# Optimization experiments

Measured on AMD Instinct MI355X. Metric: run time of the kernel, lower is better.

## Reference

```python
import jax, jax.numpy as jnp
import numpy as np
import math

B, N, L = 1, 256, 384
D_MSA, D_PAIR, H, DH = 256, 128, 8, 32


def layer_norm(x, g, b, eps=1e-5):
    m = jnp.mean(x, axis=-1, keepdims=True)
    v = jnp.var(x, axis=-1, keepdims=True)
    return (x - m) * jax.lax.rsqrt(v + eps) * g + b


def setup_inputs() -> dict:
    key = jax.random.key(0)
    ks = jax.random.split(key, 16)
    hd = H * DH
    w = lambda k, shp, s=0.05: (jax.random.normal(k, shp, dtype=jnp.float32) * s)
    return {
        "msa": jax.random.normal(ks[0], (B, N, L, D_MSA), dtype=jnp.float32),
        "pair": jax.random.normal(ks[1], (B, L, L, D_PAIR), dtype=jnp.float32),
        "ln_msa_g": jnp.ones((D_MSA,), jnp.float32),
        "ln_msa_b": jnp.zeros((D_MSA,), jnp.float32),
        "ln_pair_g": jnp.ones((D_PAIR,), jnp.float32),
        "ln_pair_b": jnp.zeros((D_PAIR,), jnp.float32),
        "sw_q_w": w(ks[2], (D_MSA, hd)),
        "sw_q_b": jnp.zeros((hd,), jnp.float32),
        "sw_k_w": w(ks[3], (D_MSA, hd)),
        "sw_k_b": jnp.zeros((hd,), jnp.float32),
        "wq": w(ks[4], (D_MSA, hd)),
        "wk": w(ks[5], (D_MSA, hd)),
        "wv": w(ks[6], (D_MSA, hd)),
        "wb": w(ks[7], (D_PAIR, H)),
        "wg": w(ks[8], (D_MSA, hd)),
        "bg": jnp.ones((hd,), jnp.float32),
        "wo": w(ks[9], (hd, D_MSA)),
        "bo": jnp.zeros((D_MSA,), jnp.float32),
    }


def reference(msa, pair, ln_msa_g, ln_msa_b, ln_pair_g, ln_pair_b,
              sw_q_w, sw_q_b, sw_k_w, sw_k_b,
              wq, wk, wv, wb, wg, bg, wo, bo):
    b, n, l, _ = msa.shape
    scale = 1.0 / math.sqrt(DH)

    msa_n = layer_norm(msa, ln_msa_g, ln_msa_b)
    pair_n = layer_norm(pair, ln_pair_g, ln_pair_b)

    # SequenceWeight: attention of target seq (row 0) over all N rows, per (L, head)
    tar = msa_n[:, 0]                                       # [B,L,D]
    swq = (tar @ sw_q_w + sw_q_b).reshape(b, l, H, DH) * scale
    swk = (msa_n @ sw_k_w + sw_k_b).reshape(b, n, l, H, DH)
    sw_logits = jnp.einsum('blhd,bnlhd->bnlh', swq, swk)    # [B,N,L,H]
    seq_weight = jax.nn.softmax(sw_logits, axis=1)          # softmax over N (dropout: eval)

    query = (msa_n @ wq).reshape(b, n, l, H, DH) * seq_weight[..., None]
    key = (msa_n @ wk).reshape(b, n, l, H, DH) * scale
    value = (msa_n @ wv).reshape(b, n, l, H, DH)
    bias = pair_n @ wb                                      # [B,L,L,H]
    gate = jax.nn.sigmoid(msa_n @ wg + bg)                  # [B,N,L,H*DH]

    attn = jnp.einsum('bsqhd,bskhd->bqkh', query, key) + bias
    attn = jax.nn.softmax(attn, axis=-2)                    # over k axis
    out = jnp.einsum('bqkh,bskhd->bsqhd', attn, value).reshape(b, n, l, H * DH)
    out = gate * out
    return out @ wo + bo
```

## Files before the change

kernel.cpp:

```cpp
#include <hip/hip_runtime.h>
#include <hip/hip_fp16.h>
#include <stdint.h>

#define NSEQ 256
#define LSEQ 384
#define DM   256
#define DP   128
#define NH   8
#define DHD  32
#define NL   (NSEQ*LSEQ)
#define LL   (LSEQ*LSEQ)
#define SCALE 0.17677669529663687f

typedef unsigned short u16;
typedef short bf16x8 __attribute__((ext_vector_type(8)));
typedef float f32x4 __attribute__((ext_vector_type(4)));

__device__ __forceinline__ float b2f(u16 s){
  union { uint32_t u; float f; } v; v.u = ((uint32_t)s)<<16; return v.f;
}
__device__ __forceinline__ u16 f2b(float f){
  union { float f; uint32_t u; } v; v.f = f;
  uint32_t u = v.u;
  return (u16)((u + 0x7FFFu + ((u>>16)&1u)) >> 16);
}
__device__ __forceinline__ uint2 pack4(float a,float b,float c,float d){
  uint2 r;
  r.x = (uint32_t)f2b(a) | ((uint32_t)f2b(b)<<16);
  r.y = (uint32_t)f2b(c) | ((uint32_t)f2b(d)<<16);
  return r;
}
__device__ __forceinline__ float wsum(float x){
  #pragma unroll
  for(int o=32;o>0;o>>=1) x += __shfl_xor(x,o,64);
  return x;
}
__device__ __forceinline__ float wmax(float x){
  #pragma unroll
  for(int o=32;o>0;o>>=1) x = fmaxf(x, __shfl_xor(x,o,64));
  return x;
}
__device__ __forceinline__ void gload16(const void* g, void* l){
  __builtin_amdgcn_global_load_lds((const __attribute__((address_space(1))) void*)g,
      (__attribute__((address_space(3))) void*)l, 16, 0, 0);
}

__global__ __launch_bounds__(256) void k_ln_msa(const float* __restrict__ msa,
    const float* __restrict__ g, const float* __restrict__ b, u16* __restrict__ out){
  int lane = threadIdx.x & 63;
  int64_t row = (int64_t)blockIdx.x*4 + (threadIdx.x>>6);
  const float4 x = *(const float4*)(msa + row*DM + lane*4);
  float s = x.x+x.y+x.z+x.w;
  float q = x.x*x.x+x.y*x.y+x.z*x.z+x.w*x.w;
  s = wsum(s); q = wsum(q);
  float mean = s*(1.0f/DM);
  float rstd = rsqrtf(q*(1.0f/DM) - mean*mean + 1e-5f);
  int c = lane*4;
  float4 gv = *(const float4*)(g+c);
  float4 bv = *(const float4*)(b+c);
  ushort4 o;
  o.x=f2b((x.x-mean)*rstd*gv.x+bv.x);
  o.y=f2b((x.y-mean)*rstd*gv.y+bv.y);
  o.z=f2b((x.z-mean)*rstd*gv.z+bv.z);
  o.w=f2b((x.w-mean)*rstd*gv.w+bv.w);
  *(ushort4*)(out + row*DM + c) = o;
}

__global__ __launch_bounds__(256) void k_wconv(const float* __restrict__ wq,
    const float* __restrict__ wk, const float* __restrict__ wv,
    const float* __restrict__ wg, const float* __restrict__ wo,
    u16* __restrict__ WTall, u16* __restrict__ WOT){
  __shared__ float tile[64][65];
  int z = blockIdx.z;
  const float* src = (z==0)?wq:(z==1)?wk:(z==2)?wv:(z==3)?wg:wo;
  u16* dst = (z<4) ? (WTall + z*DM*DM) : WOT;
  int k0 = blockIdx.x*64, n0 = blockIdx.y*64, t = threadIdx.x;
  int r = t>>4, c4 = (t&15)*4;
  #pragma unroll
  for(int it=0; it<4; it++){
    float4 v = *(const float4*)(src + (int64_t)(k0 + it*16 + r)*DM + n0 + c4);
    tile[it*16+r][c4+0]=v.x; tile[it*16+r][c4+1]=v.y;
    tile[it*16+r][c4+2]=v.z; tile[it*16+r][c4+3]=v.w;
  }
  __syncthreads();
  #pragma unroll
  for(int it=0; it<4; it++){
    int nl = it*16 + r, kl = c4;
    ushort4 o;
    o.x=f2b(tile[kl+0][nl]); o.y=f2b(tile[kl+1][nl]);
    o.z=f2b(tile[kl+2][nl]); o.w=f2b(tile[kl+3][nl]);
    *(ushort4*)(dst + (int64_t)(n0+nl)*DM + k0 + kl) = o;
  }
}

__global__ __launch_bounds__(256) void k_u(const u16* __restrict__ msa_n,
    const float* __restrict__ sw_q_w, const float* __restrict__ sw_q_b,
    const float* __restrict__ sw_k_w, float* __restrict__ u){
  __shared__ float tar[DM];
  __shared__ float swq[DM];
  int l = blockIdx.x, t = threadIdx.x;
  tar[t] = b2f(msa_n[(int64_t)l*DM + t]);
  __syncthreads();
  float acc = sw_q_b[t];
  for(int c=0;c<DM;c++) acc += tar[c]*sw_q_w[c*DM + t];
  swq[t] = acc * SCALE;
  __syncthreads();
  float res[NH];
  #pragma unroll
  for(int h=0;h<NH;h++){
    float a = 0.f;
    #pragma unroll
    for(int d=0;d<DHD;d+=4){
      float4 w = *(const float4*)(sw_k_w + t*DM + h*DHD + d);
      a += w.x*swq[h*DHD+d] + w.y*swq[h*DHD+d+1] + w.z*swq[h*DHD+d+2] + w.w*swq[h*DHD+d+3];
    }
    res[h]=a;
  }
  #pragma unroll
  for(int h=0;h<NH;h++) u[((int64_t)l*NH + h)*DM + t] = res[h];
}

__global__ __launch_bounds__(256) void k_seqw(const u16* __restrict__ msa_n,
    const float* __restrict__ u, float* __restrict__ sw){
  __shared__ float ul[NH*DM];
  __shared__ float lg[NH*256];
  __shared__ float mx[NH], sm[NH];
  int l = blockIdx.x, t = threadIdx.x;
  #pragma unroll
  for(int h=0;h<NH;h++) ul[h*DM+t] = u[((int64_t)l*NH+h)*DM + t];
  __syncthreads();
  float acc[NH] = {};
  const u16* row = msa_n + ((int64_t)t*LSEQ + l)*DM;
  for(int c=0;c<DM;c+=4){
    ushort4 xv = *(const ushort4*)(row + c);
    float x0=b2f(xv.x), x1=b2f(xv.y), x2=b2f(xv.z), x3=b2f(xv.w);
    #pragma unroll
    for(int h=0;h<NH;h++)
      acc[h] += x0*ul[h*DM+c] + x1*ul[h*DM+c+1] + x2*ul[h*DM+c+2] + x3*ul[h*DM+c+3];
  }
  #pragma unroll
  for(int h=0;h<NH;h++) lg[h*256+t] = acc[h];
  __syncthreads();
  int wv = t>>6, ln = t&63;
  for(int h=wv; h<NH; h+=4){
    float a=lg[h*256+ln], b=lg[h*256+ln+64], c=lg[h*256+ln+128], d=lg[h*256+ln+192];
    float m = wmax(fmaxf(fmaxf(a,b),fmaxf(c,d)));
    float e = __expf(a-m)+__expf(b-m)+__expf(c-m)+__expf(d-m);
    e = wsum(e);
    if(ln==0){ mx[h]=m; sm[h]=1.f/e; }
  }
  __syncthreads();
  float o[NH];
  #pragma unroll
  for(int h=0;h<NH;h++) o[h] = __expf(acc[h]-mx[h])*sm[h];
  float* dst = sw + ((int64_t)t*LSEQ + l)*NH;
  *(float4*)dst     = make_float4(o[0],o[1],o[2],o[3]);
  *(float4*)(dst+4) = make_float4(o[4],o[5],o[6],o[7]);
}

__global__ __launch_bounds__(256) void k_bias(const float* __restrict__ pair,
    const float* __restrict__ g, const float* __restrict__ b,
    const float* __restrict__ wb, float* __restrict__ bias){
  int64_t row = (int64_t)blockIdx.x*256 + threadIdx.x;
  const float* pr = pair + row*DP;
  uint2 xs[32];
  float s = 0.f, q = 0.f;
  #pragma unroll
  for(int i=0;i<32;i++){
    float4 v = *(const float4*)(pr + i*4);
    s += v.x+v.y+v.z+v.w;
    q += v.x*v.x+v.y*v.y+v.z*v.z+v.w*v.w;
    __half2 p0 = __floats2half2_rn(v.x, v.y);
    __half2 p1 = __floats2half2_rn(v.z, v.w);
    xs[i].x = *(const uint32_t*)&p0;
    xs[i].y = *(const uint32_t*)&p1;
  }
  float mean = s*(1.f/DP);
  float rstd = rsqrtf(q*(1.f/DP) - mean*mean + 1e-5f);
  float acc[NH] = {};
  #pragma unroll
  for(int i=0;i<32;i++){
    __half2 p0 = *(const __half2*)&xs[i].x;
    __half2 p1 = *(const __half2*)&xs[i].y;
    float2 f0 = __half22float2(p0);
    float2 f1 = __half22float2(p1);
    float xv[4] = {f0.x, f0.y, f1.x, f1.y};
    #pragma unroll
    for(int c4=0;c4<4;c4++){
      int c = i*4 + c4;
      float y = (xv[c4]-mean)*rstd*g[c] + b[c];
      #pragma unroll
      for(int h=0;h<NH;h++) acc[h] += y*wb[c*NH+h];
    }
  }
  #pragma unroll
  for(int h=0;h<NH;h++) bias[(int64_t)h*LL + row] = acc[h];
}


__global__ __launch_bounds__(256,2) void k_projf(const u16* __restrict__ A,
    const u16* __restrict__ WT, u16* __restrict__ qb, u16* __restrict__ kb,
    u16* __restrict__ gbuf, u16* __restrict__ VT,
    const float* __restrict__ sw, const float* __restrict__ bg){
  __shared__ short As[64*256];
  __shared__ short Bs[2][128*64];
  int t = threadIdx.x;
  int w = t>>6, lane = t&63, ln15 = lane&15, quad = lane>>4;
  int mw = (w>>1)*32, nw = (w&1)*64;
  int bx = blockIdx.x;
  int64_t r0 = (int64_t)bx*64;
  int rIn = lane>>3, cch = lane&7;
  int gB = cch ^ rIn;

  {
    int rowl = lane>>5, pc = lane&31;
    #pragma unroll
    for(int m=0;m<8;m++){
      int q = w*8+m;
      int row = 2*q + rowl;
      int gch = pc ^ (row&7);
      gload16(A + (r0+row)*DM + gch*8, &As[q*512]);
    }
  }
  #pragma unroll
  for(int m=0;m<4;m++){
    int row = w*32 + m*8 + rIn;
    gload16(WT + (int64_t)row*DM + gB*8, &Bs[0][(w*32+m*8)*64]);
  }
  __syncthreads();

  uint2 rqk[4][2][4];
  uint2 rvg[4][2][4];

  #pragma unroll
  for(int nt=0; nt<8; nt++){
    f32x4 acc[4][2] = {};
    #pragma unroll
    for(int kt=0; kt<4; kt++){
      int r = nt*4 + kt;
      int buf = r&1;
      if(r < 31){
        int rn = r+1, ntn = rn>>2, ktn = rn&3;
        #pragma unroll
        for(int m=0;m<4;m++){
          int row = w*32 + m*8 + rIn;
          gload16(WT + (int64_t)(ntn*128+row)*DM + ktn*64 + gB*8,
                  &Bs[rn&1][(w*32+m*8)*64]);
        }
      }
      #pragma unroll
      for(int ks2=0; ks2<2; ks2++){
        bf16x8 af[2], bfv[4];
        #pragma unroll
        for(int i=0;i<2;i++){
          int rw = mw+i*16+ln15;
          int ca = (kt*8 + ks2*4 + quad) ^ (rw&7);
          af[i] = *(const bf16x8*)&As[rw*256 + ca*8];
        }
        #pragma unroll
        for(int j=0;j<4;j++){
          int rw = nw+j*16+ln15;
          int cb = (ks2*4+quad) ^ (rw&7);
          bfv[j] = *(const bf16x8*)&Bs[buf][rw*64 + cb*8];
        }
        #pragma unroll
        for(int j=0;j<4;j++)
          #pragma unroll
          for(int i=0;i<2;i++)
            acc[j][i] = __builtin_amdgcn_mfma_f32_16x16x32_bf16(bfv[j], af[i], acc[j][i], 0,0,0);
      }
      if(kt==3){
        int mode = nt>>1;
        #pragma unroll
        for(int i=0;i<2;i++){
          int64_t rr = r0 + mw + i*16 + ln15;
          #pragma unroll
          for(int j=0;j<4;j++){
            int cmn = nw + j*16 + quad*4;
            float v0=acc[j][i][0], v1=acc[j][i][1], v2=acc[j][i][2], v3=acc[j][i][3];
            if(mode==0){
              float s4 = sw[rr*NH + nt*4 + (cmn>>5)];
              v0*=s4; v1*=s4; v2*=s4; v3*=s4;
            } else if(mode==1){
              v0*=SCALE; v1*=SCALE; v2*=SCALE; v3*=SCALE;
            } else if(mode==3){
              int cm0 = (nt&1)*128 + cmn;
              float4 bgv = *(const float4*)(bg + cm0);
              v0 = 1.f/(1.f+__expf(-(v0+bgv.x)));
              v1 = 1.f/(1.f+__expf(-(v1+bgv.y)));
              v2 = 1.f/(1.f+__expf(-(v2+bgv.z)));
              v3 = 1.f/(1.f+__expf(-(v3+bgv.w)));
            }
            if(nt<4) rqk[nt][i][j] = pack4(v0,v1,v2,v3);
            else     rvg[nt-4][i][j] = pack4(v0,v1,v2,v3);
          }
        }
        if(nt==3){
          #pragma unroll
          for(int n2=0;n2<4;n2++){
            u16* dst = (n2<2) ? qb : kb;
            #pragma unroll
            for(int i=0;i<2;i++){
              int64_t rr = r0 + mw + i*16 + ln15;
              #pragma unroll
              for(int j=0;j<4;j++){
                int cm0 = (n2&1)*128 + nw + j*16 + quad*4;
                *(uint2*)(dst + rr*DM + cm0) = rqk[n2][i][j];
              }
            }
          }
        }
      }
      __syncthreads();
    }
  }

  {
    int s = bx/6, kpb = (bx%6)*64;
    #pragma unroll
    for(int n2=0;n2<2;n2++){
      #pragma unroll
      for(int i=0;i<2;i++){
        int kpos = kpb + mw + i*16 + ln15;
        #pragma unroll
        for(int j=0;j<4;j++){
          int cmv = n2*128 + nw + j*16 + quad*4;
          uint2 pv = rvg[n2][i][j];
          u16 u0=(u16)(pv.x&0xffff), u1=(u16)(pv.x>>16);
          u16 u2=(u16)(pv.y&0xffff), u3=(u16)(pv.y>>16);
          int hh0 = (cmv+0)>>5, d0v = (cmv+0)&31;
          int hh1 = (cmv+1)>>5, d1v = (cmv+1)&31;
          int hh2 = (cmv+2)>>5, d2v = (cmv+2)&31;
          int hh3 = (cmv+3)>>5, d3v = (cmv+3)&31;
          VT[((int64_t)(hh0*NSEQ+s)*DHD + d0v)*LSEQ + kpos] = u0;
          VT[((int64_t)(hh1*NSEQ+s)*DHD + d1v)*LSEQ + kpos] = u1;
          VT[((int64_t)(hh2*NSEQ+s)*DHD + d2v)*LSEQ + kpos] = u2;
          VT[((int64_t)(hh3*NSEQ+s)*DHD + d3v)*LSEQ + kpos] = u3;
        }
      }
    }
    #pragma unroll
    for(int n2=2;n2<4;n2++){
      #pragma unroll
      for(int i=0;i<2;i++){
        int64_t rr = r0 + mw + i*16 + ln15;
        #pragma unroll
        for(int j=0;j<4;j++){
          int cm0 = ((n2-2)&1)*128 + nw + j*16 + quad*4;
          *(uint2*)(gbuf + rr*DM + cm0) = rvg[n2][i][j];
        }
      }
    }
  }
}

__global__ __launch_bounds__(256) void k_scores(const u16* __restrict__ Q,
    const u16* __restrict__ K, float* __restrict__ scores){
  __shared__ short As[2][128*64];
  __shared__ short Bs[2][128*64];
  int t = threadIdx.x;
  int w = t>>6, lane = t&63, ln15 = lane&15, quad = lane>>4;
  int rIn = lane>>3, cch = lane&7;
  int mw = (w>>1)*64, nw = (w&1)*64;
  int q0 = blockIdx.x*128, k0t = blockIdx.y*128;
  int h = blockIdx.z>>2, sc = blockIdx.z&3;
  int g = cch ^ rIn;
  int s_off = g>>2, d16 = g&3;

  auto STAGE = [&](int i2, int bsel){
    int sb = sc*64 + i2*2 + s_off;
    #pragma unroll
    for(int ti=0; ti<4; ti++){
      int row = w*32 + ti*8 + rIn;
      gload16(Q + ((int64_t)sb*LSEQ + q0 + row)*DM + h*DHD + d16*8, &As[bsel][(w*32+ti*8)*64]);
      gload16(K + ((int64_t)sb*LSEQ + k0t + row)*DM + h*DHD + d16*8, &Bs[bsel][(w*32+ti*8)*64]);
    }
  };

  f32x4 acc[4][4] = {};
  STAGE(0, 0);
  __syncthreads();
  for(int i2=0; i2<32; i2++){
    int buf = i2&1;
    if(i2<31) STAGE(i2+1, buf^1);
    #pragma unroll
    for(int kk=0;kk<2;kk++){
      int p = (kk*4+quad) ^ (lane&7);
      bf16x8 af[4], bfv[4];
      #pragma unroll
      for(int i=0;i<4;i++) af[i]  = *(const bf16x8*)&As[buf][(mw+i*16+ln15)*64 + p*8];
      #pragma unroll
      for(int j=0;j<4;j++) bfv[j] = *(const bf16x8*)&Bs[buf][(nw+j*16+ln15)*64 + p*8];
      #pragma unroll
      for(int i=0;i<4;i++)
        #pragma unroll
        for(int j=0;j<4;j++)
          acc[i][j] = __builtin_amdgcn_mfma_f32_16x16x32_bf16(af[i], bfv[j], acc[i][j], 0,0,0);
    }
    __syncthreads();
  }
  int64_t slab = (int64_t)sc*NH*LL;
  #pragma unroll
  for(int i=0;i<4;i++)
    #pragma unroll
    for(int reg=0;reg<4;reg++){
      int q = q0 + mw + i*16 + quad*4 + reg;
      float* rp = scores + slab + ((int64_t)h*LSEQ + q)*LSEQ + k0t + nw + ln15;
      #pragma unroll
      for(int j=0;j<4;j++) rp[j*16] = acc[i][j][reg];
    }
}

__global__ __launch_bounds__(128) void k_softmax(const float* __restrict__ scores,
    const float* __restrict__ bias, u16* __restrict__ Pb){
  int hq = blockIdx.x, t = threadIdx.x;
  int64_t base = (int64_t)hq*LSEQ;
  float v[3];
  #pragma unroll
  for(int i=0;i<3;i++){
    int k = t + i*128;
    float x = bias[base+k];
    x += scores[base+k];
    x += scores[(int64_t)1*NH*LL + base + k];
    x += scores[(int64_t)2*NH*LL + base + k];
    x += scores[(int64_t)3*NH*LL + base + k];
    v[i]=x;
  }
  __shared__ float red[2], red2[2];
  int wv=t>>6, ln=t&63;
  float m = fmaxf(fmaxf(v[0],v[1]),v[2]);
  m = wmax(m);
  if(ln==0) red[wv]=m;
  __syncthreads();
  m = fmaxf(red[0],red[1]);
  float e = __expf(v[0]-m)+__expf(v[1]-m)+__expf(v[2]-m);
  e = wsum(e);
  if(ln==0) red2[wv]=e;
  __syncthreads();
  float inv = 1.f/(red2[0]+red2[1]);
  #pragma unroll
  for(int i=0;i<3;i++) Pb[base + t + i*128] = f2b(__expf(v[i]-m)*inv);
}

__global__ __launch_bounds__(256) void k_pv(const u16* __restrict__ VT,
    const u16* __restrict__ Pb, const u16* __restrict__ gbuf,
    u16* __restrict__ attn){
  __shared__ short As[128*64];
  __shared__ short Bs[128*64];
  int t = threadIdx.x;
  int w = t>>6, lane = t&63, ln15 = lane&15, quad = lane>>4;
  int rIn = lane>>3, cch = lane&7;
  int mw = (w>>1)*64, nw = (w&1)*64;
  int mx = blockIdx.x, ny = blockIdx.y, h = blockIdx.z;
  int g = cch ^ rIn;
  f32x4 acc[4][4] = {};
  for(int it=0; it<6; it++){
    int k0 = it*64;
    __syncthreads();
    #pragma unroll
    for(int ti=0; ti<4; ti++){
      int row = w*32 + ti*8 + rIn;
      gload16(VT + ((int64_t)h*8192 + mx*128 + row)*LSEQ + k0 + g*8, &As[(w*32+ti*8)*64]);
      gload16(Pb + ((int64_t)h*LSEQ + ny*128 + row)*LSEQ + k0 + g*8, &Bs[(w*32+ti*8)*64]);
    }
    __syncthreads();
    #pragma unroll
    for(int kk=0;kk<2;kk++){
      int p = (kk*4+quad) ^ (lane&7);
      bf16x8 af[4], bfv[4];
      #pragma unroll
      for(int i=0;i<4;i++) af[i]  = *(const bf16x8*)&As[(mw+i*16+ln15)*64 + p*8];
      #pragma unroll
      for(int j=0;j<4;j++) bfv[j] = *(const bf16x8*)&Bs[(nw+j*16+ln15)*64 + p*8];
      #pragma unroll
      for(int i=0;i<4;i++)
        #pragma unroll
        for(int j=0;j<4;j++)
          acc[i][j] = __builtin_amdgcn_mfma_f32_16x16x32_bf16(af[i], bfv[j], acc[i][j], 0,0,0);
    }
  }
  #pragma unroll
  for(int i=0;i<4;i++){
    int m0 = mx*128 + mw + i*16 + quad*4;
    int s = m0>>5, d0 = m0&31;
    #pragma unroll
    for(int j=0;j<4;j++){
      int q = ny*128 + nw + j*16 + ln15;
      int64_t base = ((int64_t)s*LSEQ + q)*DM + h*DHD + d0;
      ushort4 gv = *(const ushort4*)(gbuf + base);
      ushort4 o;
      o.x = f2b(acc[i][j][0]*b2f(gv.x));
      o.y = f2b(acc[i][j][1]*b2f(gv.y));
      o.z = f2b(acc[i][j][2]*b2f(gv.z));
      o.w = f2b(acc[i][j][3]*b2f(gv.w));
      *(ushort4*)(attn + base) = o;
    }
  }
}

__global__ __launch_bounds__(256,2) void k_final(const u16* __restrict__ A,
    const u16* __restrict__ WOT, const float* __restrict__ bo,
    float* __restrict__ out){
  __shared__ short As[64*256];
  __shared__ short Bs[2][128*64];
  int t = threadIdx.x;
  int w = t>>6, lane = t&63, ln15 = lane&15, quad = lane>>4;
  int mw = (w>>1)*32, nw = (w&1)*64;
  int64_t r0 = (int64_t)blockIdx.x*64;
  int rIn = lane>>3, cch = lane&7;
  int gB = cch ^ rIn;

  {
    int rowl = lane>>5, pc = lane&31;
    #pragma unroll
    for(int m=0;m<8;m++){
      int q = w*8+m;
      int row = 2*q + rowl;
      int gch = pc ^ (row&7);
      gload16(A + (r0+row)*DM + gch*8, &As[q*512]);
    }
  }
  #pragma unroll
  for(int m=0;m<4;m++){
    int row = w*32 + m*8 + rIn;
    gload16(WOT + (int64_t)row*DM + gB*8, &Bs[0][(w*32+m*8)*64]);
  }
  __syncthreads();

  f32x4 res[2][4][2];
  #pragma unroll
  for(int nt=0; nt<2; nt++){
    f32x4 acc[4][2] = {};
    #pragma unroll
    for(int kt=0; kt<4; kt++){
      int r = nt*4 + kt;
      int buf = r&1;
      if(r < 7){
        int rn = r+1, ntn = rn>>2, ktn = rn&3;
        #pragma unroll
        for(int m=0;m<4;m++){
          int row = w*32 + m*8 + rIn;
          gload16(WOT + (int64_t)(ntn*128+row)*DM + ktn*64 + gB*8,
                  &Bs[rn&1][(w*32+m*8)*64]);
        }
      }
      #pragma unroll
      for(int ks2=0; ks2<2; ks2++){
        bf16x8 af[2], bfv[4];
        #pragma unroll
        for(int i=0;i<2;i++){
          int rw = mw+i*16+ln15;
          int ca = (kt*8 + ks2*4 + quad) ^ (rw&7);
          af[i] = *(const bf16x8*)&As[rw*256 + ca*8];
        }
        #pragma unroll
        for(int j=0;j<4;j++){
          int rw = nw+j*16+ln15;
          int cb = (ks2*4+quad) ^ (rw&7);
          bfv[j] = *(const bf16x8*)&Bs[buf][rw*64 + cb*8];
        }
        #pragma unroll
        for(int j=0;j<4;j++)
          #pragma unroll
          for(int i=0;i<2;i++)
            acc[j][i] = __builtin_amdgcn_mfma_f32_16x16x32_bf16(bfv[j], af[i], acc[j][i], 0,0,0);
      }
      __syncthreads();
    }
    #pragma unroll
    for(int j=0;j<4;j++)
      #pragma unroll
      for(int i=0;i<2;i++) res[nt][j][i] = acc[j][i];
  }

  #pragma unroll
  for(int nt=0; nt<2; nt++)
    #pragma unroll
    for(int i=0;i<2;i++){
      int64_t rr = r0 + mw + i*16 + ln15;
      #pragma unroll
      for(int j=0;j<4;j++){
        int cm0 = nt*128 + nw + j*16 + quad*4;
        float4 bv = *(const float4*)(bo + cm0);
        float4 o;
        o.x = res[nt][j][i][0] + bv.x;
        o.y = res[nt][j][i][1] + bv.y;
        o.z = res[nt][j][i][2] + bv.z;
        o.w = res[nt][j][i][3] + bv.w;
        *(float4*)(out + rr*DM + cm0) = o;
      }
    }
}

extern "C" void kernel_launch(void* const* d_in, const int* in_sizes, int n_in,
                              void* d_out, int out_size, void* d_ws, size_t ws_size,
                              hipStream_t stream){
  const float* msa    = (const float*)d_in[0];
  const float* pair   = (const float*)d_in[1];
  const float* lmg    = (const float*)d_in[2];
  const float* lmb    = (const float*)d_in[3];
  const float* lpg    = (const float*)d_in[4];
  const float* lpb    = (const float*)d_in[5];
  const float* sw_q_w = (const float*)d_in[6];
  const float* sw_q_b = (const float*)d_in[7];
  const float* sw_k_w = (const float*)d_in[8];
  const float* wq     = (const float*)d_in[10];
  const float* wk     = (const float*)d_in[11];
  const float* wv     = (const float*)d_in[12];
  const float* wb     = (const float*)d_in[13];
  const float* wg     = (const float*)d_in[14];
  const float* bg     = (const float*)d_in[15];
  const float* wo     = (const float*)d_in[16];
  const float* bo     = (const float*)d_in[17];
  float* out = (float*)d_out;

  u16* msa_n = (u16*)d_ws;
  u16* qb    = msa_n + (int64_t)NL*DM;
  u16* kb    = qb + (int64_t)NL*DM;
  u16* gbuf  = kb + (int64_t)NL*DM;
  u16* VT    = gbuf + (int64_t)NL*DM;
  u16* Pb    = VT + (int64_t)NL*DM;
  u16* WTall = Pb + (int64_t)NH*LSEQ*LSEQ;
  u16* WOT   = WTall + 1024*DM;
  float* u_buf = (float*)(WOT + DM*DM);
  float* sw  = u_buf + (int64_t)LSEQ*NH*DM;
  float* bias = sw + (int64_t)NL*NH;
  float* scores = bias + (int64_t)NH*LL;
  u16* attnout = msa_n;

  k_ln_msa<<<NL/4, 256, 0, stream>>>(msa, lmg, lmb, msa_n);
  k_wconv<<<dim3(4,4,5), 256, 0, stream>>>(wq, wk, wv, wg, wo, WTall, WOT);
  k_u<<<LSEQ, 256, 0, stream>>>(msa_n, sw_q_w, sw_q_b, sw_k_w, u_buf);
  k_seqw<<<LSEQ, 256, 0, stream>>>(msa_n, u_buf, sw);
  k_bias<<<LL/256, 256, 0, stream>>>(pair, lpg, lpb, wb, bias);
  k_projf<<<dim3(NL/64), 256, 0, stream>>>(msa_n, WTall, qb, kb, gbuf, VT, sw, bg);
  k_scores<<<dim3(3,3,32), 256, 0, stream>>>(qb, kb, scores);
  k_softmax<<<NH*LSEQ, 128, 0, stream>>>(scores, bias, Pb);
  k_pv<<<dim3(64,3,NH), 256, 0, stream>>>(VT, Pb, gbuf, attnout);
  k_final<<<dim3(NL/64), 256, 0, stream>>>(attnout, WOT, bo, out);
}
```

Measured before the change: 662.4 us.

## Triple-buffer GEMM weight tiles with vmcnt-based waits; double-buffer PV kernel

Moves the projection, scores and final GEMM kernels from double to triple buffering of LDS tiles. Prefetch now runs two stages ahead, and full __syncthreads is replaced by an s_waitcnt vmcnt(N)+s_barrier so the newest loads can stay in flight across the barrier. k_pv gains double buffering with prefetch of the next K-tile, and the q/k stores in k_projf are deferred into the next loop iteration. The aim is to hide global-load latency, at the cost of more LDS per block, which may reduce occupancy (k_scores goes to 96KB).

```diff
diff --git a/kernel.cpp b/kernel.cpp
--- a/kernel.cpp
+++ b/kernel.cpp
@@ -44,6 +44,8 @@
   __builtin_amdgcn_global_load_lds((const __attribute__((address_space(1))) void*)g,
       (__attribute__((address_space(3))) void*)l, 16, 0, 0);
 }
+
+#define WAITBAR(N) asm volatile("s_waitcnt vmcnt(" #N ")\n\ts_barrier" ::: "memory")
 
 __global__ __launch_bounds__(256) void k_ln_msa(const float* __restrict__ msa,
     const float* __restrict__ g, const float* __restrict__ b, u16* __restrict__ out){
@@ -203,7 +205,7 @@
     u16* __restrict__ gbuf, u16* __restrict__ VT,
     const float* __restrict__ sw, const float* __restrict__ bg){
   __shared__ short As[64*256];
-  __shared__ short Bs[2][128*64];
+  __shared__ short Bs[3][128*64];
   int t = threadIdx.x;
   int w = t>>6, lane = t&63, ln15 = lane&15, quad = lane>>4;
   int mw = (w>>1)*32, nw = (w&1)*64;
@@ -223,11 +225,15 @@
     }
   }
   #pragma unroll
-  for(int m=0;m<4;m++){
-    int row = w*32 + m*8 + rIn;
-    gload16(WT + (int64_t)row*DM + gB*8, &Bs[0][(w*32+m*8)*64]);
-  }
-  __syncthreads();
+  for(int rr=0;rr<2;rr++){
+    int ntn = rr>>2, ktn = rr&3;
+    #pragma unroll
+    for(int m=0;m<4;m++){
+      int row = w*32 + m*8 + rIn;
+      gload16(WT + (int64_t)(ntn*128+row)*DM + ktn*64 + gB*8, &Bs[rr][(w*32+m*8)*64]);
+    }
+  }
+  WAITBAR(4);
 
   uint2 rqk[4][2][4];
   uint2 rvg[4][2][4];
@@ -237,37 +243,53 @@
     f32x4 acc[4][2] = {};
     #pragma unroll
     for(int kt=0; kt<4; kt++){
-      int r = nt*4 + kt;
-      int buf = r&1;
-      if(r < 31){
-        int rn = r+1, ntn = rn>>2, ktn = rn&3;
+      const int r = nt*4 + kt;
+      if(nt==4 && kt==0){
+        #pragma unroll
+        for(int n2=0;n2<4;n2++){
+          u16* dst = (n2<2) ? qb : kb;
+          #pragma unroll
+          for(int i=0;i<2;i++){
+            int64_t rr = r0 + mw + i*16 + ln15;
+            #pragma unroll
+            for(int j=0;j<4;j++){
+              int cm0 = (n2&1)*128 + nw + j*16 + quad*4;
+              *(uint2*)(dst + rr*DM + cm0) = rqk[n2][i][j];
+            }
+          }
+        }
+      }
+      if(r+2 <= 31){
+        const int rn = r+2, ntn = rn>>2, ktn = rn&3, sl = rn%3;
         #pragma unroll
         for(int m=0;m<4;m++){
           int row = w*32 + m*8 + rIn;
-          gload16(WT + (int64_t)(ntn*128+row)*DM + ktn*64 + gB*8,
-                  &Bs[rn&1][(w*32+m*8)*64]);
-        }
-      }
-      #pragma unroll
-      for(int ks2=0; ks2<2; ks2++){
-        bf16x8 af[2], bfv[4];
-        #pragma unroll
-        for(int i=0;i<2;i++){
-          int rw = mw+i*16+ln15;
-          int ca = (kt*8 + ks2*4 + quad) ^ (rw&7);
-          af[i] = *(const bf16x8*)&As[rw*256 + ca*8];
-        }
-        #pragma unroll
-        for(int j=0;j<4;j++){
-          int rw = nw+j*16+ln15;
-          int cb = (ks2*4+quad) ^ (rw&7);
-          bfv[j] = *(const bf16x8*)&Bs[buf][rw*64 + cb*8];
-        }
-        #pragma unroll
-        for(int j=0;j<4;j++)
-          #pragma unroll
-          for(int i=0;i<2;i++)
-            acc[j][i] = __builtin_amdgcn_mfma_f32_16x16x32_bf16(bfv[j], af[i], acc[j][i], 0,0,0);
+          gload16(WT + (int64_t)(ntn*128+row)*DM + ktn*64 + gB*8, &Bs[sl][(w*32+m*8)*64]);
+        }
+      }
+      {
+        const int sl = r%3;
+        #pragma unroll
+        for(int ks2=0; ks2<2; ks2++){
+          bf16x8 af[2], bfv[4];
+          #pragma unroll
+          for(int i=0;i<2;i++){
+            int rw = mw+i*16+ln15;
+            int ca = (kt*8 + ks2*4 + quad) ^ (rw&7);
+            af[i] = *(const bf16x8*)&As[rw*256 + ca*8];
+          }
+          #pragma unroll
+          for(int j=0;j<4;j++){
+            int rw = nw+j*16+ln15;
+            int cb = (ks2*4+quad) ^ (rw&7);
+            bfv[j] = *(const bf16x8*)&Bs[sl][rw*64 + cb*8];
+          }
+          #pragma unroll
+          for(int j=0;j<4;j++)
+            #pragma unroll
+            for(int i=0;i<2;i++)
+              acc[j][i] = __builtin_amdgcn_mfma_f32_16x16x32_bf16(bfv[j], af[i], acc[j][i], 0,0,0);
+        }
       }
       if(kt==3){
         int mode = nt>>1;
@@ -295,23 +317,11 @@
             else     rvg[nt-4][i][j] = pack4(v0,v1,v2,v3);
           }
         }
-        if(nt==3){
-          #pragma unroll
-          for(int n2=0;n2<4;n2++){
-            u16* dst = (n2<2) ? qb : kb;
-            #pragma unroll
-            for(int i=0;i<2;i++){
-              int64_t rr = r0 + mw + i*16 + ln15;
-              #pragma unroll
-              for(int j=0;j<4;j++){
-                int cm0 = (n2&1)*128 + nw + j*16 + quad*4;
-                *(uint2*)(dst + rr*DM + cm0) = rqk[n2][i][j];
-              }
-            }
-          }
-        }
-      }
-      __syncthreads();
+      }
+      if(r < 31){
+        if(r == 30) WAITBAR(0);
+        else        WAITBAR(4);
+      }
     }
   }
 
@@ -356,8 +366,8 @@
 
 __global__ __launch_bounds__(256) void k_scores(const u16* __restrict__ Q,
     const u16* __restrict__ K, float* __restrict__ scores){
-  __shared__ short As[2][128*64];
-  __shared__ short Bs[2][128*64];
+  __shared__ short As[3][128*64];
+  __shared__ short Bs[3][128*64];
   int t = threadIdx.x;
   int w = t>>6, lane = t&63, ln15 = lane&15, quad = lane>>4;
   int rIn = lane>>3, cch = lane&7;
@@ -379,10 +389,11 @@
 
   f32x4 acc[4][4] = {};
   STAGE(0, 0);
-  __syncthreads();
+  STAGE(1, 1);
+  WAITBAR(8);
   for(int i2=0; i2<32; i2++){
-    int buf = i2&1;
-    if(i2<31) STAGE(i2+1, buf^1);
+    int buf = i2%3;
+    if(i2 < 30) STAGE(i2+2, (i2+2)%3);
     #pragma unroll
     for(int kk=0;kk<2;kk++){
       int p = (kk*4+quad) ^ (lane&7);
@@ -397,7 +408,8 @@
         for(int j=0;j<4;j++)
           acc[i][j] = __builtin_amdgcn_mfma_f32_16x16x32_bf16(af[i], bfv[j], acc[i][j], 0,0,0);
     }
-    __syncthreads();
+    if(i2 < 30)      WAITBAR(8);
+    else if(i2 == 30) WAITBAR(0);
   }
   int64_t slab = (int64_t)sc*NH*LL;
   #pragma unroll
@@ -445,39 +457,46 @@
 __global__ __launch_bounds__(256) void k_pv(const u16* __restrict__ VT,
     const u16* __restrict__ Pb, const u16* __restrict__ gbuf,
     u16* __restrict__ attn){
-  __shared__ short As[128*64];
-  __shared__ short Bs[128*64];
+  __shared__ short As[2][128*64];
+  __shared__ short Bs[2][128*64];
   int t = threadIdx.x;
   int w = t>>6, lane = t&63, ln15 = lane&15, quad = lane>>4;
   int rIn = lane>>3, cch = lane&7;
   int mw = (w>>1)*64, nw = (w&1)*64;
   int mx = blockIdx.x, ny = blockIdx.y, h = blockIdx.z;
   int g = cch ^ rIn;
-  f32x4 acc[4][4] = {};
-  for(int it=0; it<6; it++){
+
+  auto STAGE = [&](int it, int bsel){
     int k0 = it*64;
-    __syncthreads();
     #pragma unroll
     for(int ti=0; ti<4; ti++){
       int row = w*32 + ti*8 + rIn;
-      gload16(VT + ((int64_t)h*8192 + mx*128 + row)*LSEQ + k0 + g*8, &As[(w*32+ti*8)*64]);
-      gload16(Pb + ((int64_t)h*LSEQ + ny*128 + row)*LSEQ + k0 + g*8, &Bs[(w*32+ti*8)*64]);
-    }
-    __syncthreads();
+      gload16(VT + ((int64_t)h*8192 + mx*128 + row)*LSEQ + k0 + g*8, &As[bsel][(w*32+ti*8)*64]);
+      gload16(Pb + ((int64_t)h*LSEQ + ny*128 + row)*LSEQ + k0 + g*8, &Bs[bsel][(w*32+ti*8)*64]);
+    }
+  };
+
+  f32x4 acc[4][4] = {};
+  STAGE(0, 0);
+  __syncthreads();
+  for(int it=0; it<6; it++){
+    int buf = it&1;
+    if(it<5) STAGE(it+1, buf^1);
     #pragma unroll
     for(int kk=0;kk<2;kk++){
       int p = (kk*4+quad) ^ (lane&7);
       bf16x8 af[4], bfv[4];
       #pragma unroll
-      for(int i=0;i<4;i++) af[i]  = *(const bf16x8*)&As[(mw+i*16+ln15)*64 + p*8];
-      #pragma unroll
-      for(int j=0;j<4;j++) bfv[j] = *(const bf16x8*)&Bs[(nw+j*16+ln15)*64 + p*8];
+      for(int i=0;i<4;i++) af[i]  = *(const bf16x8*)&As[buf][(mw+i*16+ln15)*64 + p*8];
+      #pragma unroll
+      for(int j=0;j<4;j++) bfv[j] = *(const bf16x8*)&Bs[buf][(nw+j*16+ln15)*64 + p*8];
       #pragma unroll
       for(int i=0;i<4;i++)
         #pragma unroll
         for(int j=0;j<4;j++)
           acc[i][j] = __builtin_amdgcn_mfma_f32_16x16x32_bf16(af[i], bfv[j], acc[i][j], 0,0,0);
     }
+    __syncthreads();
   }
   #pragma unroll
   for(int i=0;i<4;i++){
@@ -502,7 +521,7 @@
     const u16* __restrict__ WOT, const float* __restrict__ bo,
     float* __restrict__ out){
   __shared__ short As[64*256];
-  __shared__ short Bs[2][128*64];
+  __shared__ short Bs[3][128*64];
   int t = threadIdx.x;
   int w = t>>6, lane = t&63, ln15 = lane&15, quad = lane>>4;
   int mw = (w>>1)*32, nw = (w&1)*64;
@@ -521,11 +540,15 @@
     }
   }
   #pragma unroll
-  for(int m=0;m<4;m++){
-    int row = w*32 + m*8 + rIn;
-    gload16(WOT + (int64_t)row*DM + gB*8, &Bs[0][(w*32+m*8)*64]);
-  }
-  __syncthreads();
+  for(int rr=0;rr<2;rr++){
+    int ntn = rr>>2, ktn = rr&3;
+    #pragma unroll
+    for(int m=0;m<4;m++){
+      int row = w*32 + m*8 + rIn;
+      gload16(WOT + (int64_t)(ntn*128+row)*DM + ktn*64 + gB*8, &Bs[rr][(w*32+m*8)*64]);
+    }
+  }
+  WAITBAR(4);
 
   f32x4 res[2][4][2];
   #pragma unroll
@@ -533,39 +556,43 @@
     f32x4 acc[4][2] = {};
     #pragma unroll
     for(int kt=0; kt<4; kt++){
-      int r = nt*4 + kt;
-      int buf = r&1;
-      if(r < 7){
-        int rn = r+1, ntn = rn>>2, ktn = rn&3;
+      const int r = nt*4 + kt;
+      if(r+2 <= 7){
+        const int rn = r+2, ntn = rn>>2, ktn = rn&3, sl = rn%3;
         #pragma unroll
         for(int m=0;m<4;m++){
           int row = w*32 + m*8 + rIn;
-          gload16(WOT + (int64_t)(ntn*128+row)*DM + ktn*64 + gB*8,
-                  &Bs[rn&1][(w*32+m*8)*64]);
-        }
-      }
-      #pragma unroll
-      for(int ks2=0; ks2<2; ks2++){
-        bf16x8 af[2], bfv[4];
-        #pragma unroll
-        for(int i=0;i<2;i++){
-          int rw = mw+i*16+ln15;
-          int ca = (kt*8 + ks2*4 + quad) ^ (rw&7);
-          af[i] = *(const bf16x8*)&As[rw*256 + ca*8];
-        }
-        #pragma unroll
-        for(int j=0;j<4;j++){
-          int rw = nw+j*16+ln15;
-          int cb = (ks2*4+quad) ^ (rw&7);
-          bfv[j] = *(const bf16x8*)&Bs[buf][rw*64 + cb*8];
-        }
-        #pragma unroll
-        for(int j=0;j<4;j++)
-          #pragma unroll
-          for(int i=0;i<2;i++)
-            acc[j][i] = __builtin_amdgcn_mfma_f32_16x16x32_bf16(bfv[j], af[i], acc[j][i], 0,0,0);
-      }
-      __syncthreads();
+          gload16(WOT + (int64_t)(ntn*128+row)*DM + ktn*64 + gB*8, &Bs[sl][(w*32+m*8)*64]);
+        }
+      }
+      {
+        const int sl = r%3;
+        #pragma unroll
+        for(int ks2=0; ks2<2; ks2++){
+          bf16x8 af[2], bfv[4];
+          #pragma unroll
+          for(int i=0;i<2;i++){
+            int rw = mw+i*16+ln15;
+            int ca = (kt*8 + ks2*4 + quad) ^ (rw&7);
+            af[i] = *(const bf16x8*)&As[rw*256 + ca*8];
+          }
+          #pragma unroll
+          for(int j=0;j<4;j++){
+            int rw = nw+j*16+ln15;
+            int cb = (ks2*4+quad) ^ (rw&7);
+            bfv[j] = *(const bf16x8*)&Bs[sl][rw*64 + cb*8];
+          }
+          #pragma unroll
+          for(int j=0;j<4;j++)
+            #pragma unroll
+            for(int i=0;i<2;i++)
+              acc[j][i] = __builtin_amdgcn_mfma_f32_16x16x32_bf16(bfv[j], af[i], acc[j][i], 0,0,0);
+        }
+      }
+      if(r < 7){
+        if(r == 6) WAITBAR(0);
+        else       WAITBAR(4);
+      }
     }
     #pragma unroll
     for(int j=0;j<4;j++)
```

New measurement: 661.1 us. Within noise of the previous version (-0.2%).
